# Performance work log

Hardware: AMD Instinct MI355X
Metric: run time of the kernel (lower is better)

## Reference

```python
import jax, jax.numpy as jnp
import numpy as np


def setup_inputs() -> dict:
    key = jax.random.key(0)
    ks = jax.random.split(key, 12)
    N_DRUGS, D, N_CELLS, C_IN, E = 4096, 128, 1024, 1000, 500000
    inp = {
        "drug_hidden_out": jax.random.normal(ks[0], (N_DRUGS, D), dtype=jnp.float32),
        "cell_hidden_out": jax.random.normal(ks[1], (N_CELLS, C_IN), dtype=jnp.float32),
        # columns: drug1_idx, drug2_idx, cell_idx, label (original code indexes
        # drug_hidden_out with ALL THREE index columns, so bound by N_DRUGS)
        "all_edges": jax.random.randint(ks[2], (E, 4), 0, N_DRUGS, dtype=jnp.int64),
        # proj: Linear(1000, 128)
        "proj_W": jax.random.normal(ks[3], (D, C_IN), dtype=jnp.float32) * 0.03,
        "proj_b": jnp.zeros((D,), dtype=jnp.float32),
        # NN: Linear(128,32) -> ReLU -> Linear(32,32) -> ReLU -> Linear(32,32)
        #     -> ReLU -> Dropout(eval=identity) -> Linear(32,1) -> Sigmoid
        "W1": jax.random.normal(ks[4], (32, D), dtype=jnp.float32) * 0.08,
        "b1": jnp.zeros((32,), dtype=jnp.float32),
        "W2": jax.random.normal(ks[5], (32, 32), dtype=jnp.float32) * 0.17,
        "b2": jnp.zeros((32,), dtype=jnp.float32),
        "W3": jax.random.normal(ks[6], (32, 32), dtype=jnp.float32) * 0.17,
        "b3": jnp.zeros((32,), dtype=jnp.float32),
        "W4": jax.random.normal(ks[7], (1, 32), dtype=jnp.float32) * 0.17,
        "b4": jnp.zeros((1,), dtype=jnp.float32),
    }
    return inp


def reference(drug_hidden_out, cell_hidden_out, all_edges,
              proj_W, proj_b, W1, b1, W2, b2, W3, b3, W4, b4):
    # proj is computed in the original forward but its result is never used
    # downstream (the code re-indexes drug_hidden_out for cell_fea).
    _cell_proj = cell_hidden_out @ proj_W.T + proj_b  # [n_cells, 128], dead value

    edges = all_edges.T                 # [4, E]
    label = edges[3]                    # [E]
    edge_index = edges[:3]              # [3, E]

    drug1_fea = drug_hidden_out[edge_index[0]]   # [E, 128] gather
    drug2_fea = drug_hidden_out[edge_index[1]]   # [E, 128] gather
    cell_fea = drug_hidden_out[edge_index[2]]    # [E, 128] gather (faithful to source bug)
    logits = drug1_fea * drug2_fea * cell_fea    # [E, 128]

    h = jax.nn.relu(logits @ W1.T + b1)          # [E, 32]
    h = jax.nn.relu(h @ W2.T + b2)               # [E, 32]
    h = jax.nn.relu(h @ W3.T + b3)               # [E, 32] (dropout = identity in eval)
    x = jax.nn.sigmoid(h @ W4.T + b4)            # [E, 1]
    return x, label
```

## Files before the change

kernel.cpp:

```cpp
#include <hip/hip_runtime.h>
#include <stdint.h>

#define DD 128
#define HH 32
#define TABQ (4096 * DD / 4)
#define BLOB_OFF (1u << 20)

typedef _Float16 f16;
typedef _Float16 f16x2 __attribute__((ext_vector_type(2)));
typedef _Float16 f16x4 __attribute__((ext_vector_type(4)));
typedef _Float16 f16x8 __attribute__((ext_vector_type(8)));
typedef float    f32x4 __attribute__((ext_vector_type(4)));
typedef uint32_t u32x4 __attribute__((ext_vector_type(4)));

__global__ __launch_bounds__(256)
void synergy_prepass(const float* __restrict__ drug,
                     const float* __restrict__ W1, const float* __restrict__ W2,
                     const float* __restrict__ W3, const float* __restrict__ W4,
                     f16* __restrict__ tab)
{
    const int tid = threadIdx.x;
    if ((int)blockIdx.x == 512) {
        f16x8* __restrict__ blob16 = (f16x8*)((char*)tab + BLOB_OFF);
        const float4* __restrict__ W1v = (const float4*)W1;
        #pragma unroll
        for (int p = 0; p < 2; ++p) {
            const int S = p * 256 + tid;
            const int t = S >> 8, f = (S >> 6) & 3, l = S & 63;
            const int mm = l & 15, qq = l >> 4;
            const int c4 = (t * 16 + mm) * (DD / 4) + f * 8 + qq * 2;
            const float4 w0 = W1v[c4], w1 = W1v[c4 + 1];
            f16x8 r;
            r[0]=(f16)w0.x; r[1]=(f16)w0.y; r[2]=(f16)w0.z; r[3]=(f16)w0.w;
            r[4]=(f16)w1.x; r[5]=(f16)w1.y; r[6]=(f16)w1.z; r[7]=(f16)w1.w;
            blob16[S] = r;
        }
        {
            const int B = tid & 127;
            const int t = B >> 6, l = B & 63;
            const int mm = l & 15, qq = l >> 4;
            const int c4 = (t * 16 + mm) * (HH / 4) + qq * 2;
            const float4* __restrict__ src = (tid < 128) ? (const float4*)W2 : (const float4*)W3;
            const float4 w0 = src[c4], w1 = src[c4 + 1];
            f16x8 r;
            r[0]=(f16)w0.x; r[1]=(f16)w0.y; r[2]=(f16)w0.z; r[3]=(f16)w0.w;
            r[4]=(f16)w1.x; r[5]=(f16)w1.y; r[6]=(f16)w1.z; r[7]=(f16)w1.w;
            blob16[512 + (tid & 128) + B] = r;
        }
        if (tid < 64) {
            const int mm = tid & 15, qq = tid >> 4;
            f16x8 r;
            #pragma unroll
            for (int j = 0; j < 8; ++j)
                r[j] = (mm == 0) ? (f16)W4[qq * 8 + j] : (f16)0.0f;
            blob16[768 + tid] = r;
        }
        return;
    }
    const int i = blockIdx.x * 256 + tid;
    if (i < TABQ) {
        const float4 v = ((const float4*)drug)[i];
        f16x4 h;
        h[0]=(f16)v.x; h[1]=(f16)v.y; h[2]=(f16)v.z; h[3]=(f16)v.w;
        ((f16x4*)tab)[i] = h;
    }
}

static __device__ __forceinline__ uint32_t pkh(float a, float b) {
    f16x2 h; h[0] = (f16)a; h[1] = (f16)b;
    return __builtin_bit_cast(uint32_t, h);
}
static __device__ __forceinline__ void plswap32(uint32_t &a, uint32_t &b) {
#if __has_builtin(__builtin_amdgcn_permlane32_swap)
    auto r = __builtin_amdgcn_permlane32_swap(a, b, false, false);
    a = r[0]; b = r[1];
#else
    asm volatile("v_permlane32_swap_b32 %0, %1" : "+v"(a), "+v"(b));
#endif
}
static __device__ __forceinline__ void plswap16(uint32_t &a, uint32_t &b) {
#if __has_builtin(__builtin_amdgcn_permlane16_swap)
    auto r = __builtin_amdgcn_permlane16_swap(a, b, false, false);
    a = r[0]; b = r[1];
#else
    asm volatile("v_permlane16_swap_b32 %0, %1" : "+v"(a), "+v"(b));
#endif
}

static __device__ __forceinline__ void pin4(f16x8 &w) {
    u32x4 t = __builtin_bit_cast(u32x4, w);
    asm volatile("" : "+v"(t));
    w = __builtin_bit_cast(f16x8, t);
}

static __device__ __forceinline__ f16x8 transition(f32x4 a0, f32x4 a1) {
    uint32_t u0 = pkh(fmaxf(a0[0], 0.f), fmaxf(a0[1], 0.f));
    uint32_t u1 = pkh(fmaxf(a0[2], 0.f), fmaxf(a0[3], 0.f));
    uint32_t v0 = pkh(fmaxf(a1[0], 0.f), fmaxf(a1[1], 0.f));
    uint32_t v1 = pkh(fmaxf(a1[2], 0.f), fmaxf(a1[3], 0.f));
    plswap32(u0, v0);
    plswap32(u1, v1);
    plswap16(u0, v0);
    plswap16(u1, v1);
    u32x4 d; d[0] = u0; d[1] = u1; d[2] = v0; d[3] = v1;
    return __builtin_bit_cast(f16x8, d);
}

__global__ __launch_bounds__(256, 3)
void synergy_main(const f16* __restrict__ tab, const int* __restrict__ edges,
                  const float* __restrict__ b1, const float* __restrict__ b2,
                  const float* __restrict__ b3, const float* __restrict__ b4,
                  float* __restrict__ out, int E, int NG)
{
    __shared__ __align__(16) float blds[96];

    const int tid  = threadIdx.x;
    const int wave = tid >> 6;
    const int lane = tid & 63;
    const int m    = lane & 15;
    const int q    = lane >> 4;

    const char* __restrict__ tabB   = (const char*)tab;
    const f16x8* __restrict__ blobG = (const f16x8*)(tabB + BLOB_OFF);

    if (tid < 96) {
        const float* __restrict__ src = (tid < 32) ? b1 : ((tid < 64) ? b2 : b3);
        blds[tid] = src[tid & 31];
    }
    __syncthreads();

    const int WSTR = (int)gridDim.x * 4;
    int g = (int)blockIdx.x * 4 + wave;
    if (g >= NG) return;

    f16x8 w1a[4], w1b[4];
    #pragma unroll
    for (int f = 0; f < 4; ++f) {
        w1a[f] = blobG[f * 64 + lane];
        w1b[f] = blobG[256 + f * 64 + lane];
    }
    f16x8 w2a = blobG[512 + lane], w2b = blobG[576 + lane];
    f16x8 w3a = blobG[640 + lane], w3b = blobG[704 + lane];
    f16x8 wf4 = blobG[768 + lane];
    #pragma unroll
    for (int f = 0; f < 4; ++f) { pin4(w1a[f]); pin4(w1b[f]); }
    pin4(w2a); pin4(w2b); pin4(w3a); pin4(w3b); pin4(wf4);
    const float b4v = b4[0];

    const int4* __restrict__ edges4 = (const int4*)edges;

    auto load_ed = [&](int gg) -> int4 {
        int e = (gg << 4) + m;
        e = (e < E) ? e : (E - 1);
        return edges4[e];
    };

    f16x8 v[4][3];
    auto issue_gather = [&](const int4 ed) {
        const char* __restrict__ p0 = tabB + ((ed.x << 8) | (q << 4));
        const char* __restrict__ p1 = tabB + ((ed.y << 8) | (q << 4));
        const char* __restrict__ p2 = tabB + ((ed.z << 8) | (q << 4));
        #pragma unroll
        for (int f = 0; f < 4; ++f) {
            v[f][0] = *(const f16x8*)(p0 + f * 64);
            v[f][1] = *(const f16x8*)(p1 + f * 64);
            v[f][2] = *(const f16x8*)(p2 + f * 64);
        }
    };

    int4 ed_cur = load_ed(g);
    issue_gather(ed_cur);
    int gn = g + WSTR;
    int4 ed_nxt = load_ed((gn < NG) ? gn : g);

    int wzero = 0;
    for (;;) {
        asm volatile("" : "+v"(wzero));
        const f32x4* __restrict__ bl = (const f32x4*)blds + wzero;

        f32x4 acc0 = bl[q];
        f32x4 acc1 = bl[4 + q];
        #pragma unroll
        for (int f = 0; f < 4; ++f) {
            const f16x8 p = v[f][0] * v[f][1] * v[f][2];
            acc0 = __builtin_amdgcn_mfma_f32_16x16x32_f16(w1a[f], p, acc0, 0, 0, 0);
            acc1 = __builtin_amdgcn_mfma_f32_16x16x32_f16(w1b[f], p, acc1, 0, 0, 0);
        }
        const f16x8 h1 = transition(acc0, acc1);

        const bool last = (gn >= NG);
        int4 ed_fut = ed_nxt;
        if (!last) {
            issue_gather(ed_nxt);
            const int gf = gn + WSTR;
            ed_fut = load_ed((gf < NG) ? gf : g);
        }

        f32x4 c0 = bl[8 + q];
        f32x4 c1 = bl[12 + q];
        c0 = __builtin_amdgcn_mfma_f32_16x16x32_f16(w2a, h1, c0, 0, 0, 0);
        c1 = __builtin_amdgcn_mfma_f32_16x16x32_f16(w2b, h1, c1, 0, 0, 0);
        const f16x8 h2 = transition(c0, c1);

        f32x4 d0 = bl[16 + q];
        f32x4 d1 = bl[20 + q];
        d0 = __builtin_amdgcn_mfma_f32_16x16x32_f16(w3a, h2, d0, 0, 0, 0);
        d1 = __builtin_amdgcn_mfma_f32_16x16x32_f16(w3b, h2, d1, 0, 0, 0);
        const f16x8 h3 = transition(d0, d1);

        {
            f32x4 z = {b4v, b4v, b4v, b4v};
            z = __builtin_amdgcn_mfma_f32_16x16x32_f16(wf4, h3, z, 0, 0, 0);
            if (q == 0) {
                const int e0 = (g << 4) + m;
                if (e0 < E) out[e0] = 1.0f / (1.0f + __expf(-z[0]));
            }
        }
        const int eL = (g << 4) + lane;
        if (lane < 16 && eL < E) out[E + eL] = (float)ed_cur.w;

        if (last) break;
        g = gn; gn += WSTR; ed_cur = ed_nxt; ed_nxt = ed_fut;
    }
}

extern "C" void kernel_launch(void* const* d_in, const int* in_sizes, int n_in,
                              void* d_out, int out_size, void* d_ws, size_t ws_size,
                              hipStream_t stream)
{
    const float* drug  = (const float*)d_in[0];
    const int*   edges = (const int*)d_in[2];
    const float* W1 = (const float*)d_in[5];
    const float* b1 = (const float*)d_in[6];
    const float* W2 = (const float*)d_in[7];
    const float* b2 = (const float*)d_in[8];
    const float* W3 = (const float*)d_in[9];
    const float* b3 = (const float*)d_in[10];
    const float* W4 = (const float*)d_in[11];
    const float* b4 = (const float*)d_in[12];
    float* out = (float*)d_out;
    f16*   tab = (f16*)d_ws;

    const int E  = in_sizes[2] / 4;
    const int NG = (E + 15) / 16;

    hipLaunchKernelGGL(synergy_prepass, dim3(513), dim3(256), 0, stream,
                       drug, W1, W2, W3, W4, tab);
    int blocks = (NG + 3) / 4;
    if (blocks > 768) blocks = 768;
    hipLaunchKernelGGL(synergy_main, dim3(blocks), dim3(256), 0, stream,
                       tab, edges, b1, b2, b3, b4, out, E, NG);
}
```

Baseline: 135.6 us.

## Gather drug rows via direct global-to-LDS DMA with swizzled staging

Replaces the per-lane register gathers of the three drug rows with global_load_lds transfers into a per-wave LDS staging buffer, using a rotated 16-byte segment layout to avoid bank conflicts. The operands are then read back from LDS before the W1 MFMAs. The next tile's DMA is issued only after the current tile's output is written, because the single staging buffer per wave is reused. This removes register pressure from the in-flight gathers, but the prefetch overlap shrinks and it adds a waitcnt plus 48KB of LDS per block, which may cut occupancy.

```diff
diff --git a/kernel.cpp b/kernel.cpp
--- a/kernel.cpp
+++ b/kernel.cpp
@@ -12,6 +12,9 @@
 typedef _Float16 f16x8 __attribute__((ext_vector_type(8)));
 typedef float    f32x4 __attribute__((ext_vector_type(4)));
 typedef uint32_t u32x4 __attribute__((ext_vector_type(4)));
+
+#define GL1(p)  ((const __attribute__((address_space(1))) void*)(p))
+#define LDS3(p) ((__attribute__((address_space(3))) void*)(p))
 
 __global__ __launch_bounds__(256)
 void synergy_prepass(const float* __restrict__ drug,
@@ -112,6 +115,7 @@
                   const float* __restrict__ b3, const float* __restrict__ b4,
                   float* __restrict__ out, int E, int NG)
 {
+    __shared__ __align__(16) f16 stage[4][6144];
     __shared__ __align__(16) float blds[96];
 
     const int tid  = threadIdx.x;
@@ -147,6 +151,7 @@
     pin4(w2a); pin4(w2b); pin4(w3a); pin4(w3b); pin4(wf4);
     const float b4v = b4[0];
 
+    f16* __restrict__ stg = stage[wave];
     const int4* __restrict__ edges4 = (const int4*)edges;
 
     auto load_ed = [&](int gg) -> int4 {
@@ -154,27 +159,36 @@
         e = (e < E) ? e : (E - 1);
         return edges4[e];
     };
-
-    f16x8 v[4][3];
-    auto issue_gather = [&](const int4 ed) {
-        const char* __restrict__ p0 = tabB + ((ed.x << 8) | (q << 4));
-        const char* __restrict__ p1 = tabB + ((ed.y << 8) | (q << 4));
-        const char* __restrict__ p2 = tabB + ((ed.z << 8) | (q << 4));
-        #pragma unroll
-        for (int f = 0; f < 4; ++f) {
-            v[f][0] = *(const f16x8*)(p0 + f * 64);
-            v[f][1] = *(const f16x8*)(p1 + f * 64);
-            v[f][2] = *(const f16x8*)(p2 + f * 64);
-        }
+    auto issue_dma = [&](const int4 ed) {
+        int rowb[12];
+        #pragma unroll
+        for (int gg = 0; gg < 4; ++gg) {
+            const int src = 4 * gg + q;
+            rowb[0 * 4 + gg] = __shfl(ed.x, src, 64) << 8;
+            rowb[1 * 4 + gg] = __shfl(ed.y, src, 64) << 8;
+            rowb[2 * 4 + gg] = __shfl(ed.z, src, 64) << 8;
+        }
+        __builtin_amdgcn_sched_barrier(0);
+        #pragma unroll
+        for (int t = 0; t < 3; ++t)
+            #pragma unroll
+            for (int gg = 0; gg < 4; ++gg) {
+                const int seg16 = ((m + 4 * gg + q) & 15) << 4;
+                __builtin_amdgcn_global_load_lds(
+                    GL1(tabB + (size_t)(rowb[t * 4 + gg] + seg16)),
+                    LDS3((char*)stg + (t * 16 + 4 * gg) * 256), 16, 0, 0);
+            }
     };
 
     int4 ed_cur = load_ed(g);
-    issue_gather(ed_cur);
+    issue_dma(ed_cur);
     int gn = g + WSTR;
     int4 ed_nxt = load_ed((gn < NG) ? gn : g);
 
     int wzero = 0;
     for (;;) {
+        __builtin_amdgcn_s_waitcnt(0x0F70);
+        __builtin_amdgcn_sched_barrier(0);
         asm volatile("" : "+v"(wzero));
         const f32x4* __restrict__ bl = (const f32x4*)blds + wzero;
 
@@ -182,19 +196,18 @@
         f32x4 acc1 = bl[4 + q];
         #pragma unroll
         for (int f = 0; f < 4; ++f) {
-            const f16x8 p = v[f][0] * v[f][1] * v[f][2];
+            const int slot = (((f * 4 + q) - m) & 15) << 3;
+            const f16x8 v0 = *(const f16x8*)(stg + (0 * 16 + m) * 128 + slot);
+            const f16x8 v1 = *(const f16x8*)(stg + (1 * 16 + m) * 128 + slot);
+            const f16x8 v2 = *(const f16x8*)(stg + (2 * 16 + m) * 128 + slot);
+            const f16x8 p = v0 * v1 * v2;
             acc0 = __builtin_amdgcn_mfma_f32_16x16x32_f16(w1a[f], p, acc0, 0, 0, 0);
             acc1 = __builtin_amdgcn_mfma_f32_16x16x32_f16(w1b[f], p, acc1, 0, 0, 0);
         }
         const f16x8 h1 = transition(acc0, acc1);
 
-        const bool last = (gn >= NG);
-        int4 ed_fut = ed_nxt;
-        if (!last) {
-            issue_gather(ed_nxt);
-            const int gf = gn + WSTR;
-            ed_fut = load_ed((gf < NG) ? gf : g);
-        }
+        const int gf = gn + WSTR;
+        const int4 ed_fut = load_ed((gf < NG) ? gf : g);
 
         f32x4 c0 = bl[8 + q];
         f32x4 c1 = bl[12 + q];
@@ -219,8 +232,9 @@
         const int eL = (g << 4) + lane;
         if (lane < 16 && eL < E) out[E + eL] = (float)ed_cur.w;
 
-        if (last) break;
-        g = gn; gn += WSTR; ed_cur = ed_nxt; ed_nxt = ed_fut;
+        if (gn >= NG) break;
+        issue_dma(ed_nxt);
+        g = gn; gn = gf; ed_cur = ed_nxt; ed_nxt = ed_fut;
     }
 }
 
```

Measured after the change: 114.6 us. 1.18x faster.
